# Kernel optimization log

Hardware: AMD Instinct MI355X
Metric: run time of the kernel (lower is better)

## Reference

```python
import jax, jax.numpy as jnp
import numpy as np

D_FEAT = 6
HIDDEN = 64
NEG_SLOPE = 0.01  # torch LeakyReLU default


def gru_layer(x, Wih, Whh, bih, bhh):
    # x: [N, T, D] -> outputs [N, T, H], PyTorch GRU gate math (r,z,n order)
    N = x.shape[0]
    H = Whh.shape[1]
    def step(h, xt):
        gi = xt @ Wih.T + bih          # [N, 3H]
        gh = h @ Whh.T + bhh           # [N, 3H]
        i_r, i_z, i_n = jnp.split(gi, 3, axis=-1)
        h_r, h_z, h_n = jnp.split(gh, 3, axis=-1)
        r = jax.nn.sigmoid(i_r + h_r)
        z = jax.nn.sigmoid(i_z + h_z)
        n = jnp.tanh(i_n + r * h_n)
        h_new = (1.0 - z) * n + z * h
        return h_new, h_new
    h0 = jnp.zeros((N, H), x.dtype)
    _, hs = jax.lax.scan(step, h0, jnp.swapaxes(x, 0, 1))  # hs: [T, N, H]
    return jnp.swapaxes(hs, 0, 1)


def setup_inputs() -> dict:
    key = jax.random.key(0)
    ks = jax.random.split(key, 16)
    N, T, D, H, R = 2048, 60, D_FEAT, HIDDEN, 20
    x = jax.random.normal(ks[0], (N, D * T), dtype=jnp.float32)
    vals = jax.random.uniform(ks[1], (N, N, R), dtype=jnp.float32)
    keep = jax.random.uniform(ks[2], (N, N, R), dtype=jnp.float32) < 0.3
    relation_matrix = vals * keep.astype(jnp.float32)
    s = 1.0 / np.sqrt(H)
    def u(k, shape):
        return jax.random.uniform(k, shape, dtype=jnp.float32, minval=-s, maxval=s)
    inp = {
        "x": x,
        "relation_matrix": relation_matrix,
        "Wih0": u(ks[3], (3 * H, D)),
        "Whh0": u(ks[4], (3 * H, H)),
        "bih0": u(ks[5], (3 * H,)),
        "bhh0": u(ks[6], (3 * H,)),
        "Wih1": u(ks[7], (3 * H, H)),
        "Whh1": u(ks[8], (3 * H, H)),
        "bih1": u(ks[9], (3 * H,)),
        "bhh1": u(ks[10], (3 * H,)),
        "W": jax.random.normal(ks[11], (2 * H + R, 1), dtype=jnp.float32) * 0.1,
        "b": jnp.zeros((1,), dtype=jnp.float32),
        "fc_w": u(ks[12], (1, H)),
        "fc_b": jnp.zeros((1,), dtype=jnp.float32),
    }
    return inp


def reference(x, relation_matrix, Wih0, Whh0, bih0, bhh0, Wih1, Whh1, bih1, bhh1, W, b, fc_w, fc_b):
    N = x.shape[0]
    H = HIDDEN
    R = relation_matrix.shape[2]
    # [N, d_feat*T] -> [N, T, d_feat]
    xs = jnp.transpose(x.reshape(N, D_FEAT, -1), (0, 2, 1))
    h = gru_layer(xs, Wih0, Whh0, bih0, bhh0)
    h = gru_layer(h, Wih1, Whh1, bih1, bhh1)
    x_hidden = h[:, -1, :]  # [N, H]
    # decompose concat @ W:  W = [W1 (ei part); W2 (hidden part); W3 (relation part)]
    W1 = W[:H, 0]
    W2 = W[H:2 * H, 0]
    W3 = W[2 * H:, 0]
    ai = x_hidden @ W1          # [N] contribution of row i
    aj = x_hidden @ W2          # [N] contribution of col j
    ar = jnp.einsum('ijr,r->ij', relation_matrix, W3)  # [N, N]
    weight = ai[:, None] + aj[None, :] + ar + b[0]
    weight = jnp.where(weight >= 0, weight, NEG_SLOPE * weight)  # leaky_relu
    mask = (jnp.sum(relation_matrix, axis=2) != 0).astype(x_hidden.dtype)
    valid_weight = mask * weight
    valid_weight = jax.nn.softmax(valid_weight, axis=1)
    hidden = valid_weight @ x_hidden  # [N, H]
    pred_all = ((hidden + x_hidden) @ fc_w.T + fc_b).squeeze(-1)  # [N]
    return pred_all
```

## Files before the change

### kernel.cpp

```cpp
#include <hip/hip_runtime.h>
#include <cstddef>

typedef __attribute__((ext_vector_type(8))) short short8;
typedef __attribute__((ext_vector_type(4))) float f32x4;

#define MFMA16(a, b, c) __builtin_amdgcn_mfma_f32_16x16x32_bf16((a), (b), (c), 0, 0, 0)

__device__ __forceinline__ unsigned short f2bf(float f) {
    unsigned u = __float_as_uint(f);
    u = (u + 0x7fffu + ((u >> 16) & 1u)) >> 16;
    return (unsigned short)u;
}
__device__ __forceinline__ float bf2f(unsigned short s) {
    return __uint_as_float(((unsigned)s) << 16);
}
__device__ __forceinline__ float sigm(float v) { return 1.f / (1.f + __expf(-v)); }
__device__ __forceinline__ float tanh_(float v) {
    float a = fabsf(v);
    float e = __expf(-2.f * a);
    float t = (1.f - e) / (1.f + e);
    return v < 0.f ? -t : t;
}

__device__ __forceinline__ void lds_order_fence() {
    asm volatile("" ::: "memory");
    __builtin_amdgcn_sched_barrier(0);
}

__launch_bounds__(768, 3)
__global__ void gru_kernel(const float* __restrict__ x,
                           const float* __restrict__ Wih0, const float* __restrict__ Whh0,
                           const float* __restrict__ bih0, const float* __restrict__ bhh0,
                           const float* __restrict__ Wih1, const float* __restrict__ Whh1,
                           const float* __restrict__ bih1, const float* __restrict__ bhh1,
                           float* __restrict__ xhid) {
    __shared__ __align__(16) unsigned short h0h[2][1024], h0l[2][1024];
    __shared__ __align__(16) unsigned short h1h[2][1024], h1l[2][1024];
    __shared__ __align__(16) float P1[2][16][195];
    __shared__ __align__(16) short8 axbuf[2400];

    const int tid  = threadIdx.x;
    const int grp  = tid >> 8;
    const int lane = tid & 63;
    const int gw   = (tid >> 6) & 3;
    const int c    = lane & 15;
    const int q    = lane >> 4;
    const int jj   = gw * 16 + c;

    for (int i = tid; i < 1024; i += 768) {
        h0h[0][i] = 0; h0l[0][i] = 0; h1h[0][i] = 0; h1l[0][i] = 0;
    }
    {
        const float* xb = x + (size_t)blockIdx.x * 8 * 360;
        for (int f = tid; f < 1920; f += 768) {
            const int t = f >> 5, s = (f >> 2) & 7, qq = f & 3;
            unsigned short Hh[6], Ll[6];
#pragma unroll
            for (int d = 0; d < 6; ++d) {
                const float v = xb[s * 360 + d * 60 + t];
                Hh[d] = f2bf(v); Ll[d] = f2bf(v - bf2f(Hh[d]));
            }
            short8 fr;
#pragma unroll
            for (int e = 0; e < 8; ++e) {
                const int k = qq * 8 + e;
                unsigned short u = 0;
                if (k < 6) u = Hh[k];
                else if (k < 12) u = Ll[k - 6];
                else if (k < 18) u = Hh[k - 12];
                fr[e] = (short)u;
            }
            axbuf[t * 40 + s * 5 + qq] = fr;
        }
    }

    const int ka    = q * 8;
    const int swzA0 = c * 64 + (ka ^ ((c & 7) << 3));
    const int swzA1 = c * 64 + ((32 + ka) ^ ((c & 7) << 3));

    __syncthreads();

    if (grp == 0) {
        short8 Bhh[3][2], Bhl[3][2], Bc[3];
#pragma unroll
        for (int g = 0; g < 3; ++g) {
            const int o = g * 64 + jj;
#pragma unroll
            for (int kt = 0; kt < 2; ++kt) {
                const int k0 = kt * 32 + q * 8;
#pragma unroll
                for (int e = 0; e < 8; ++e) {
                    const float v = Whh0[o * 64 + k0 + e];
                    const unsigned short hi = f2bf(v);
                    Bhh[g][kt][e] = (short)hi; Bhl[g][kt][e] = (short)f2bf(v - bf2f(hi));
                }
            }
#pragma unroll
            for (int e = 0; e < 8; ++e) {
                const int ks = q * 8 + e;
                unsigned short bv = 0;
                if (ks < 6)       bv = f2bf(Wih0[o * 6 + ks]);
                else if (ks < 12) bv = f2bf(Wih0[o * 6 + ks - 6]);
                else if (ks < 18) {
                    const float v = Wih0[o * 6 + ks - 12];
                    const unsigned short hi = f2bf(v);
                    bv = f2bf(v - bf2f(hi));
                }
                Bc[g][e] = (short)bv;
            }
        }
        const float br = bih0[jj] + bhh0[jj];
        const float bz = bih0[64 + jj] + bhh0[64 + jj];
        const float bi = bih0[128 + jj];
        const float bh = bhh0[128 + jj];
        float hreg[4] = {0.f, 0.f, 0.f, 0.f};

        for (int it = 0; it < 62; ++it) {
            if (it < 60) {
                const int par = it & 1;
                const short8 ah0 = *(const short8*)&h0h[par][swzA0];
                const short8 ah1 = *(const short8*)&h0h[par][swzA1];
                const short8 al0 = *(const short8*)&h0l[par][swzA0];
                const short8 al1 = *(const short8*)&h0l[par][swzA1];
                const short8 ax  = axbuf[it * 40 + (c & 7) * 5 + q];

                f32x4 accr = {br, br, br, br};
                f32x4 accz = {bz, bz, bz, bz};
                f32x4 acci = {bi, bi, bi, bi};
                f32x4 acch = {bh, bh, bh, bh};

                accr = MFMA16(ah0, Bhh[0][0], accr); accr = MFMA16(ah1, Bhh[0][1], accr);
                accr = MFMA16(al0, Bhh[0][0], accr); accr = MFMA16(al1, Bhh[0][1], accr);
                accr = MFMA16(ah0, Bhl[0][0], accr); accr = MFMA16(ah1, Bhl[0][1], accr);
                accr = MFMA16(ax, Bc[0], accr);

                accz = MFMA16(ah0, Bhh[1][0], accz); accz = MFMA16(ah1, Bhh[1][1], accz);
                accz = MFMA16(al0, Bhh[1][0], accz); accz = MFMA16(al1, Bhh[1][1], accz);
                accz = MFMA16(ah0, Bhl[1][0], accz); accz = MFMA16(ah1, Bhl[1][1], accz);
                accz = MFMA16(ax, Bc[1], accz);

                acci = MFMA16(ax, Bc[2], acci);

                acch = MFMA16(ah0, Bhh[2][0], acch); acch = MFMA16(ah1, Bhh[2][1], acch);
                acch = MFMA16(al0, Bhh[2][0], acch); acch = MFMA16(al1, Bhh[2][1], acch);
                acch = MFMA16(ah0, Bhl[2][0], acch); acch = MFMA16(ah1, Bhl[2][1], acch);

#pragma unroll
                for (int i2 = 0; i2 < 4; ++i2) {
                    const float rr = sigm(accr[i2]);
                    const float zz = sigm(accz[i2]);
                    const float nn = tanh_(acci[i2] + rr * acch[i2]);
                    const float hv = (1.f - zz) * nn + zz * hreg[i2];
                    hreg[i2] = hv;
                    const int r  = q * 4 + i2;
                    const int ix = r * 64 + (jj ^ ((r & 7) << 3));
                    const unsigned short hi = f2bf(hv);
                    h0h[par ^ 1][ix] = hi;
                    h0l[par ^ 1][ix] = f2bf(hv - bf2f(hi));
                }
            }
            __syncthreads();
        }
    } else if (grp == 1) {
        short8 Bih[3][2], Bil[3][2];
#pragma unroll
        for (int g = 0; g < 3; ++g) {
            const int o = g * 64 + jj;
#pragma unroll
            for (int kt = 0; kt < 2; ++kt) {
                const int k0 = kt * 32 + q * 8;
#pragma unroll
                for (int e = 0; e < 8; ++e) {
                    const float v = Wih1[o * 64 + k0 + e];
                    const unsigned short hi = f2bf(v);
                    Bih[g][kt][e] = (short)hi; Bil[g][kt][e] = (short)f2bf(v - bf2f(hi));
                }
            }
        }
        const float br = bih1[jj] + bhh1[jj];
        const float bz = bih1[64 + jj] + bhh1[64 + jj];
        const float bi = bih1[128 + jj];

        for (int it = 0; it < 62; ++it) {
            if (it >= 1 && it < 61) {
                const int par = it & 1;
                const short8 gh0 = *(const short8*)&h0h[par][swzA0];
                const short8 gh1 = *(const short8*)&h0h[par][swzA1];
                const short8 gl0 = *(const short8*)&h0l[par][swzA0];
                const short8 gl1 = *(const short8*)&h0l[par][swzA1];

                f32x4 ar = {br, br, br, br};
                f32x4 az = {bz, bz, bz, bz};
                f32x4 an = {bi, bi, bi, bi};

                ar = MFMA16(gh0, Bih[0][0], ar); ar = MFMA16(gh1, Bih[0][1], ar);
                ar = MFMA16(gl0, Bih[0][0], ar); ar = MFMA16(gl1, Bih[0][1], ar);
                ar = MFMA16(gh0, Bil[0][0], ar); ar = MFMA16(gh1, Bil[0][1], ar);

                az = MFMA16(gh0, Bih[1][0], az); az = MFMA16(gh1, Bih[1][1], az);
                az = MFMA16(gl0, Bih[1][0], az); az = MFMA16(gl1, Bih[1][1], az);
                az = MFMA16(gh0, Bil[1][0], az); az = MFMA16(gh1, Bil[1][1], az);

                an = MFMA16(gh0, Bih[2][0], an); an = MFMA16(gh1, Bih[2][1], an);
                an = MFMA16(gl0, Bih[2][0], an); an = MFMA16(gl1, Bih[2][1], an);
                an = MFMA16(gh0, Bil[2][0], an); an = MFMA16(gh1, Bil[2][1], an);

#pragma unroll
                for (int i2 = 0; i2 < 4; ++i2) {
                    const int r = q * 4 + i2;
                    P1[par][r][jj]       = ar[i2];
                    P1[par][r][64 + jj]  = az[i2];
                    P1[par][r][128 + jj] = an[i2];
                }
            }
            __syncthreads();
        }
    } else {
        short8 Bhh[3][2], Bhl[3][2];
#pragma unroll
        for (int g = 0; g < 3; ++g) {
            const int o = g * 64 + jj;
#pragma unroll
            for (int kt = 0; kt < 2; ++kt) {
                const int k0 = kt * 32 + q * 8;
#pragma unroll
                for (int e = 0; e < 8; ++e) {
                    const float v = Whh1[o * 64 + k0 + e];
                    const unsigned short hi = f2bf(v);
                    Bhh[g][kt][e] = (short)hi; Bhl[g][kt][e] = (short)f2bf(v - bf2f(hi));
                }
            }
        }
        const float bh = bhh1[128 + jj];
        float hreg[4] = {0.f, 0.f, 0.f, 0.f};

        for (int it = 0; it < 62; ++it) {
            if (it >= 2) {
                const int par = it & 1;
                const short8 hh0 = *(const short8*)&h1h[par][swzA0];
                const short8 hh1_ = *(const short8*)&h1h[par][swzA1];
                const short8 hl0 = *(const short8*)&h1l[par][swzA0];
                const short8 hl1_ = *(const short8*)&h1l[par][swzA1];

                float p1r[4], p1z[4], p1n[4];
#pragma unroll
                for (int i2 = 0; i2 < 4; ++i2) {
                    const int r = q * 4 + i2;
                    p1r[i2] = P1[par ^ 1][r][jj];
                    p1z[i2] = P1[par ^ 1][r][64 + jj];
                    p1n[i2] = P1[par ^ 1][r][128 + jj];
                }

                f32x4 ar  = {p1r[0], p1r[1], p1r[2], p1r[3]};
                f32x4 az  = {p1z[0], p1z[1], p1z[2], p1z[3]};
                f32x4 ahn = {bh, bh, bh, bh};

                ar = MFMA16(hh0, Bhh[0][0], ar); ar = MFMA16(hh1_, Bhh[0][1], ar);
                ar = MFMA16(hl0, Bhh[0][0], ar); ar = MFMA16(hl1_, Bhh[0][1], ar);
                ar = MFMA16(hh0, Bhl[0][0], ar); ar = MFMA16(hh1_, Bhl[0][1], ar);

                az = MFMA16(hh0, Bhh[1][0], az); az = MFMA16(hh1_, Bhh[1][1], az);
                az = MFMA16(hl0, Bhh[1][0], az); az = MFMA16(hl1_, Bhh[1][1], az);
                az = MFMA16(hh0, Bhl[1][0], az); az = MFMA16(hh1_, Bhl[1][1], az);

                ahn = MFMA16(hh0, Bhh[2][0], ahn); ahn = MFMA16(hh1_, Bhh[2][1], ahn);
                ahn = MFMA16(hl0, Bhh[2][0], ahn); ahn = MFMA16(hl1_, Bhh[2][1], ahn);
                ahn = MFMA16(hh0, Bhl[2][0], ahn); ahn = MFMA16(hh1_, Bhl[2][1], ahn);

#pragma unroll
                for (int i2 = 0; i2 < 4; ++i2) {
                    const float rr = sigm(ar[i2]);
                    const float zz = sigm(az[i2]);
                    const float nn = tanh_(p1n[i2] + rr * ahn[i2]);
                    const float hv = (1.f - zz) * nn + zz * hreg[i2];
                    hreg[i2] = hv;
                    const int r  = q * 4 + i2;
                    const int ix = r * 64 + (jj ^ ((r & 7) << 3));
                    const unsigned short hi = f2bf(hv);
                    h1h[par ^ 1][ix] = hi;
                    h1l[par ^ 1][ix] = f2bf(hv - bf2f(hi));
                    if (it == 61 && q < 2)
                        xhid[((size_t)blockIdx.x * 8 + r) * 64 + jj] = hv;
                }
            }
            __syncthreads();
        }
    }
}

__global__ void aij_kernel(const float* __restrict__ xh, const float* __restrict__ W,
                           float* __restrict__ ai, float* __restrict__ aj) {
    const int n = blockIdx.x * 256 + threadIdx.x;
    const float* row = xh + (size_t)n * 64;
    float a1 = 0.f, a2 = 0.f;
#pragma unroll
    for (int k = 0; k < 64; k += 4) {
        const f32x4 v = *(const f32x4*)(row + k);
#pragma unroll
        for (int u = 0; u < 4; ++u) {
            a1 += v[u] * W[k + u];
            a2 += v[u] * W[64 + k + u];
        }
    }
    ai[n] = a1;
    aj[n] = a2;
}

__launch_bounds__(1024, 2)
__global__ void relfused_kernel(const float* __restrict__ rel, const float* __restrict__ xh,
                                const float* __restrict__ ai, const float* __restrict__ aj,
                                const float* __restrict__ W, const float* __restrict__ bptr,
                                const float* __restrict__ fcw, const float* __restrict__ fcb,
                                float* __restrict__ out) {
    __shared__ __align__(16) float sc[8][2056];
    __shared__ __align__(16) float scratch[16][1280];
    __shared__ float redm[8][2], reds[8][2], rinv_s[8];

    const int tid  = threadIdx.x;
    const int lane = tid & 63;
    const int wvA  = tid >> 6;
    const int i0   = blockIdx.x * 8;

    float w3[20];
#pragma unroll
    for (int e = 0; e < 20; ++e) w3[e] = W[128 + e];
    const float bb = bptr[0];
    float* b = scratch[wvA];

    f32x4 A0, A1, A2, A3, A4, B0, B1, B2, B3, B4;

#define REL_ISSUE(tk, R0, R1, R2, R3, R4)                                        \
    {                                                                            \
        const int task_ = wvA * 16 + (tk);                                       \
        const int il_ = task_ >> 5, ch_ = task_ & 31;                            \
        const float* gp = rel + ((size_t)(i0 + il_) * 2048 + ch_ * 64) * 20      \
                          + lane * 4;                                            \
        R0 = *(const f32x4*)(gp);                                                \
        R1 = *(const f32x4*)(gp + 256);                                          \
        R2 = *(const f32x4*)(gp + 512);                                          \
        R3 = *(const f32x4*)(gp + 768);                                          \
        R4 = *(const f32x4*)(gp + 1024);                                         \
    }

#define REL_CONSUME(tk, R0, R1, R2, R3, R4)                                      \
    {                                                                            \
        const int task_ = wvA * 16 + (tk);                                       \
        const int il_ = task_ >> 5, ch_ = task_ & 31;                            \
        *(f32x4*)&b[0    + lane * 4] = R0;                                       \
        *(f32x4*)&b[256  + lane * 4] = R1;                                       \
        *(f32x4*)&b[512  + lane * 4] = R2;                                       \
        *(f32x4*)&b[768  + lane * 4] = R3;                                       \
        *(f32x4*)&b[1024 + lane * 4] = R4;                                       \
        lds_order_fence();                  \
        float arv = 0.f, ms = 0.f;                                               \
        _Pragma("unroll")                                                        \
        for (int e = 0; e < 5; ++e) {                                            \
            const f32x4 v = *(const f32x4*)&b[lane * 20 + e * 4];                \
            arv += v[0] * w3[e * 4] + v[1] * w3[e * 4 + 1]                       \
                 + v[2] * w3[e * 4 + 2] + v[3] * w3[e * 4 + 3];                  \
            ms  += v[0] + v[1] + v[2] + v[3];                                    \
        }                                                                        \
        lds_order_fence();             \
        const int j_ = ch_ * 64 + lane;                                          \
        float wvv = ai[i0 + il_] + aj[j_] + arv + bb;                            \
        wvv = (wvv >= 0.f) ? wvv : 0.01f * wvv;                                  \
        sc[il_][j_] = (ms != 0.f) ? wvv : 0.f;                                   \
    }

    REL_ISSUE(0, A0, A1, A2, A3, A4);
    for (int t = 0; t < 16; ++t) {
        if ((t & 1) == 0) {
            if (t < 15) REL_ISSUE(t + 1, B0, B1, B2, B3, B4);
            REL_CONSUME(t, A0, A1, A2, A3, A4);
        } else {
            if (t < 15) REL_ISSUE(t + 1, A0, A1, A2, A3, A4);
            REL_CONSUME(t, B0, B1, B2, B3, B4);
        }
    }
    __syncthreads();

    const int row = tid >> 7;
    const int c7  = tid & 127;
    const int wh  = (tid >> 6) & 1;

    float mx = -1e30f;
#pragma unroll
    for (int m = 0; m < 16; ++m) mx = fmaxf(mx, sc[row][c7 + 128 * m]);
#pragma unroll
    for (int d = 1; d < 64; d <<= 1) mx = fmaxf(mx, __shfl_xor(mx, d, 64));
    if ((tid & 63) == 0) redm[row][wh] = mx;
    __syncthreads();
    mx = fmaxf(redm[row][0], redm[row][1]);

    float sm = 0.f;
#pragma unroll
    for (int m = 0; m < 16; ++m) {
        const int k = c7 + 128 * m;
        const float e = __expf(sc[row][k] - mx);
        sc[row][k] = e;
        sm += e;
    }
#pragma unroll
    for (int d = 1; d < 64; d <<= 1) sm += __shfl_xor(sm, d, 64);
    if ((tid & 63) == 0) reds[row][wh] = sm;
    __syncthreads();
    if ((tid & 127) == 0) rinv_s[row] = 1.f / (reds[row][0] + reds[row][1]);

    float (*hidpart)[8][64] = (float (*)[8][64])scratch;
    const int col   = tid & 63;
    const int strip = tid >> 6;
    const int k0s   = strip * 128;

    float acc[8] = {0.f, 0.f, 0.f, 0.f, 0.f, 0.f, 0.f, 0.f};
    for (int k = 0; k < 128; k += 4) {
        const float v0 = xh[(size_t)(k0s + k) * 64 + col];
        const float v1 = xh[(size_t)(k0s + k + 1) * 64 + col];
        const float v2 = xh[(size_t)(k0s + k + 2) * 64 + col];
        const float v3 = xh[(size_t)(k0s + k + 3) * 64 + col];
#pragma unroll
        for (int il = 0; il < 8; ++il) {
            const f32x4 e = *(const f32x4*)&sc[il][k0s + k];
            acc[il] += e[0] * v0 + e[1] * v1 + e[2] * v2 + e[3] * v3;
        }
    }
#pragma unroll
    for (int il = 0; il < 8; ++il) hidpart[strip][il][col] = acc[il];
    __syncthreads();

    if (tid < 512) {
        const int r2 = tid >> 6;
        const int cl = tid & 63;
        float hsum = 0.f;
#pragma unroll
        for (int s = 0; s < 16; ++s) hsum += hidpart[s][r2][cl];
        const float h = hsum * rinv_s[r2] + xh[(size_t)(i0 + r2) * 64 + cl];
        float p = h * fcw[cl];
#pragma unroll
        for (int d = 1; d < 64; d <<= 1) p += __shfl_xor(p, d, 64);
        if (cl == 0) out[i0 + r2] = p + fcb[0];
    }
}

extern "C" void kernel_launch(void* const* d_in, const int* in_sizes, int n_in,
                              void* d_out, int out_size, void* d_ws, size_t ws_size,
                              hipStream_t stream) {
    const float* x    = (const float*)d_in[0];
    const float* rel  = (const float*)d_in[1];
    const float* Wih0 = (const float*)d_in[2];
    const float* Whh0 = (const float*)d_in[3];
    const float* bih0 = (const float*)d_in[4];
    const float* bhh0 = (const float*)d_in[5];
    const float* Wih1 = (const float*)d_in[6];
    const float* Whh1 = (const float*)d_in[7];
    const float* bih1 = (const float*)d_in[8];
    const float* bhh1 = (const float*)d_in[9];
    const float* W    = (const float*)d_in[10];
    const float* b    = (const float*)d_in[11];
    const float* fcw  = (const float*)d_in[12];
    const float* fcb  = (const float*)d_in[13];
    float* out = (float*)d_out;

    float* xh = (float*)d_ws;
    float* ai = xh + 2048 * 64;
    float* aj = ai + 2048;

    gru_kernel<<<256, 768, 0, stream>>>(x, Wih0, Whh0, bih0, bhh0,
                                        Wih1, Whh1, bih1, bhh1, xh);
    aij_kernel<<<8, 256, 0, stream>>>(xh, W, ai, aj);
    relfused_kernel<<<256, 1024, 0, stream>>>(rel, xh, ai, aj, W, b, fcw, fcb, out);
}
```

Before: 177.1 us.

## Overlap relation-tensor reduction with GRU in a merged heterogeneous kernel

The GRU kernel and the relation-tensor reduction now share one launch. Extra blocks stream the whole relation tensor, computing the per-pair relation score and a ballot-packed nonzero mask into workspace while the GRU blocks run. The bandwidth-heavy relation read, which previously waited for the latency-bound GRU, can now overlap with it, and a lighter finish kernel only reads the compact intermediates. In exchange, the GRU kernel's LDS footprint grows to the merged buffer size, which may reduce occupancy, and a score array and mask array are added to workspace traffic.

```diff
diff --git a/kernel.cpp b/kernel.cpp
--- a/kernel.cpp
+++ b/kernel.cpp
@@ -28,24 +28,94 @@
 }
 
 __launch_bounds__(768, 3)
-__global__ void gru_kernel(const float* __restrict__ x,
-                           const float* __restrict__ Wih0, const float* __restrict__ Whh0,
-                           const float* __restrict__ bih0, const float* __restrict__ bhh0,
-                           const float* __restrict__ Wih1, const float* __restrict__ Whh1,
-                           const float* __restrict__ bih1, const float* __restrict__ bhh1,
-                           float* __restrict__ xhid) {
-    __shared__ __align__(16) unsigned short h0h[2][1024], h0l[2][1024];
-    __shared__ __align__(16) unsigned short h1h[2][1024], h1l[2][1024];
-    __shared__ __align__(16) float P1[2][16][195];
-    __shared__ __align__(16) short8 axbuf[2400];
+__global__ void mega_kernel(const float* __restrict__ x,
+                            const float* __restrict__ Wih0, const float* __restrict__ Whh0,
+                            const float* __restrict__ bih0, const float* __restrict__ bhh0,
+                            const float* __restrict__ Wih1, const float* __restrict__ Whh1,
+                            const float* __restrict__ bih1, const float* __restrict__ bhh1,
+                            const float* __restrict__ rel, const float* __restrict__ W,
+                            float* __restrict__ xhid, float* __restrict__ arw,
+                            unsigned long long* __restrict__ maskw) {
+    __shared__ __align__(16) unsigned char smem[79744];
 
     const int tid  = threadIdx.x;
+    const int lane = tid & 63;
+
+    if (blockIdx.x >= 256) {
+        const int bid = blockIdx.x - 256;
+        const int wv  = tid >> 6;
+        const int gw  = bid * 12 + wv;
+        float* b = (float*)smem + wv * 1280;
+
+        float w3[20];
+#pragma unroll
+        for (int e = 0; e < 20; ++e) w3[e] = W[128 + e];
+
+        f32x4 A0, A1, A2, A3, A4, B0, B1, B2, B3, B4;
+
+#define REL_ISSUE(tsk, R0, R1, R2, R3, R4)                                       \
+    {                                                                            \
+        const float* gp = rel + (size_t)(tsk) * 1280 + lane * 4;                 \
+        R0 = *(const f32x4*)(gp);                                                \
+        R1 = *(const f32x4*)(gp + 256);                                          \
+        R2 = *(const f32x4*)(gp + 512);                                          \
+        R3 = *(const f32x4*)(gp + 768);                                          \
+        R4 = *(const f32x4*)(gp + 1024);                                         \
+    }
+
+#define REL_CONSUME(tsk, R0, R1, R2, R3, R4)                                     \
+    {                                                                            \
+        *(f32x4*)&b[0    + lane * 4] = R0;                                       \
+        *(f32x4*)&b[256  + lane * 4] = R1;                                       \
+        *(f32x4*)&b[512  + lane * 4] = R2;                                       \
+        *(f32x4*)&b[768  + lane * 4] = R3;                                       \
+        *(f32x4*)&b[1024 + lane * 4] = R4;                                       \
+        lds_order_fence();                              \
+        float arv = 0.f, ms = 0.f;                                               \
+        _Pragma("unroll")                                                        \
+        for (int e = 0; e < 5; ++e) {                                            \
+            const f32x4 v = *(const f32x4*)&b[lane * 20 + e * 4];                \
+            arv += v[0] * w3[e * 4] + v[1] * w3[e * 4 + 1]                       \
+                 + v[2] * w3[e * 4 + 2] + v[3] * w3[e * 4 + 3];                  \
+            ms  += v[0] + v[1] + v[2] + v[3];                                    \
+        }                                                                        \
+        lds_order_fence();             \
+        arw[(size_t)(tsk) * 64 + lane] = arv;                                    \
+        const unsigned long long bal = __ballot(ms != 0.f);                      \
+        if (lane == 0) maskw[tsk] = bal;                                         \
+    }
+
+        int t = gw, k = 0;
+        REL_ISSUE(t, A0, A1, A2, A3, A4);
+        while (t < 65536) {
+            const int tn = t + 9216;
+            if ((k & 1) == 0) {
+                if (tn < 65536) REL_ISSUE(tn, B0, B1, B2, B3, B4);
+                REL_CONSUME(t, A0, A1, A2, A3, A4);
+            } else {
+                if (tn < 65536) REL_ISSUE(tn, A0, A1, A2, A3, A4);
+                REL_CONSUME(t, B0, B1, B2, B3, B4);
+            }
+            t = tn; ++k;
+        }
+#undef REL_ISSUE
+#undef REL_CONSUME
+        return;
+    }
+
+    typedef unsigned short ush;
+    ush (*h0h)[1024] = (ush (*)[1024])(smem);
+    ush (*h0l)[1024] = (ush (*)[1024])(smem + 4096);
+    ush (*h1h)[1024] = (ush (*)[1024])(smem + 8192);
+    ush (*h1l)[1024] = (ush (*)[1024])(smem + 12288);
+    float (*P1)[16][195] = (float (*)[16][195])(smem + 16384);
+    short8* axbuf = (short8*)(smem + 41344);
+
     const int grp  = tid >> 8;
-    const int lane = tid & 63;
-    const int gw   = (tid >> 6) & 3;
+    const int gw_  = (tid >> 6) & 3;
     const int c    = lane & 15;
     const int q    = lane >> 4;
-    const int jj   = gw * 16 + c;
+    const int jj   = gw_ * 16 + c;
 
     for (int i = tid; i < 1024; i += 768) {
         h0h[0][i] = 0; h0l[0][i] = 0; h1h[0][i] = 0; h1l[0][i] = 0;
@@ -307,74 +377,35 @@
 }
 
 __launch_bounds__(1024, 2)
-__global__ void relfused_kernel(const float* __restrict__ rel, const float* __restrict__ xh,
-                                const float* __restrict__ ai, const float* __restrict__ aj,
-                                const float* __restrict__ W, const float* __restrict__ bptr,
-                                const float* __restrict__ fcw, const float* __restrict__ fcb,
-                                float* __restrict__ out) {
+__global__ void finish_kernel(const float* __restrict__ arw,
+                              const unsigned long long* __restrict__ maskw,
+                              const float* __restrict__ xh, const float* __restrict__ ai,
+                              const float* __restrict__ aj, const float* __restrict__ bptr,
+                              const float* __restrict__ fcw, const float* __restrict__ fcb,
+                              float* __restrict__ out) {
     __shared__ __align__(16) float sc[8][2056];
-    __shared__ __align__(16) float scratch[16][1280];
+    __shared__ __align__(16) float hidpart[16][8][64];
     __shared__ float redm[8][2], reds[8][2], rinv_s[8];
 
-    const int tid  = threadIdx.x;
-    const int lane = tid & 63;
-    const int wvA  = tid >> 6;
-    const int i0   = blockIdx.x * 8;
-
-    float w3[20];
-#pragma unroll
-    for (int e = 0; e < 20; ++e) w3[e] = W[128 + e];
+    const int tid = threadIdx.x;
+    const int i0  = blockIdx.x * 8;
+
+    float aiv[8];
+#pragma unroll
+    for (int il = 0; il < 8; ++il) aiv[il] = ai[i0 + il];
     const float bb = bptr[0];
-    float* b = scratch[wvA];
-
-    f32x4 A0, A1, A2, A3, A4, B0, B1, B2, B3, B4;
-
-#define REL_ISSUE(tk, R0, R1, R2, R3, R4)                                        \
-    {                                                                            \
-        const int task_ = wvA * 16 + (tk);                                       \
-        const int il_ = task_ >> 5, ch_ = task_ & 31;                            \
-        const float* gp = rel + ((size_t)(i0 + il_) * 2048 + ch_ * 64) * 20      \
-                          + lane * 4;                                            \
-        R0 = *(const f32x4*)(gp);                                                \
-        R1 = *(const f32x4*)(gp + 256);                                          \
-        R2 = *(const f32x4*)(gp + 512);                                          \
-        R3 = *(const f32x4*)(gp + 768);                                          \
-        R4 = *(const f32x4*)(gp + 1024);                                         \
-    }
-
-#define REL_CONSUME(tk, R0, R1, R2, R3, R4)                                      \
-    {                                                                            \
-        const int task_ = wvA * 16 + (tk);                                       \
-        const int il_ = task_ >> 5, ch_ = task_ & 31;                            \
-        *(f32x4*)&b[0    + lane * 4] = R0;                                       \
-        *(f32x4*)&b[256  + lane * 4] = R1;                                       \
-        *(f32x4*)&b[512  + lane * 4] = R2;                                       \
-        *(f32x4*)&b[768  + lane * 4] = R3;                                       \
-        *(f32x4*)&b[1024 + lane * 4] = R4;                                       \
-        lds_order_fence();                  \
-        float arv = 0.f, ms = 0.f;                                               \
-        _Pragma("unroll")                                                        \
-        for (int e = 0; e < 5; ++e) {                                            \
-            const f32x4 v = *(const f32x4*)&b[lane * 20 + e * 4];                \
-            arv += v[0] * w3[e * 4] + v[1] * w3[e * 4 + 1]                       \
-                 + v[2] * w3[e * 4 + 2] + v[3] * w3[e * 4 + 3];                  \
-            ms  += v[0] + v[1] + v[2] + v[3];                                    \
-        }                                                                        \
-        lds_order_fence();             \
-        const int j_ = ch_ * 64 + lane;                                          \
-        float wvv = ai[i0 + il_] + aj[j_] + arv + bb;                            \
-        wvv = (wvv >= 0.f) ? wvv : 0.01f * wvv;                                  \
-        sc[il_][j_] = (ms != 0.f) ? wvv : 0.f;                                   \
-    }
-
-    REL_ISSUE(0, A0, A1, A2, A3, A4);
-    for (int t = 0; t < 16; ++t) {
-        if ((t & 1) == 0) {
-            if (t < 15) REL_ISSUE(t + 1, B0, B1, B2, B3, B4);
-            REL_CONSUME(t, A0, A1, A2, A3, A4);
-        } else {
-            if (t < 15) REL_ISSUE(t + 1, A0, A1, A2, A3, A4);
-            REL_CONSUME(t, B0, B1, B2, B3, B4);
+
+#pragma unroll
+    for (int jc = 0; jc < 2; ++jc) {
+        const int j = tid + jc * 1024;
+        const float ajv = aj[j];
+#pragma unroll
+        for (int il = 0; il < 8; ++il) {
+            const float s = arw[(size_t)(i0 + il) * 2048 + j];
+            const unsigned long long mw = maskw[(size_t)(i0 + il) * 32 + (j >> 6)];
+            float wvv = aiv[il] + ajv + s + bb;
+            wvv = (wvv >= 0.f) ? wvv : 0.01f * wvv;
+            sc[il][j] = ((mw >> (j & 63)) & 1ull) ? wvv : 0.f;
         }
     }
     __syncthreads();
@@ -406,7 +437,6 @@
     __syncthreads();
     if ((tid & 127) == 0) rinv_s[row] = 1.f / (reds[row][0] + reds[row][1]);
 
-    float (*hidpart)[8][64] = (float (*)[8][64])scratch;
     const int col   = tid & 63;
     const int strip = tid >> 6;
     const int k0s   = strip * 128;
@@ -461,11 +491,14 @@
     float* out = (float*)d_out;
 
     float* xh = (float*)d_ws;
-    float* ai = xh + 2048 * 64;
+    float* ai = xh + 131072;
     float* aj = ai + 2048;
-
-    gru_kernel<<<256, 768, 0, stream>>>(x, Wih0, Whh0, bih0, bhh0,
-                                        Wih1, Whh1, bih1, bhh1, xh);
+    float* arw = aj + 2048;
+    unsigned long long* maskw = (unsigned long long*)(arw + 4194304);
+
+    mega_kernel<<<1024, 768, 0, stream>>>(x, Wih0, Whh0, bih0, bhh0,
+                                          Wih1, Whh1, bih1, bhh1,
+                                          rel, W, xh, arw, maskw);
     aij_kernel<<<8, 256, 0, stream>>>(xh, W, ai, aj);
-    relfused_kernel<<<256, 1024, 0, stream>>>(rel, xh, ai, aj, W, b, fcw, fcb, out);
-}
+    finish_kernel<<<256, 1024, 0, stream>>>(arw, maskw, xh, ai, aj, b, fcw, fcb, out);
+}
```

After: 188.0 us. 6.1% more time.
